# Optimization experiments

Hardware: AMD Instinct MI355X
Metric: run time of the kernel (lower is better)

The kernel has to match this reference:

```python
import jax, jax.numpy as jnp
import numpy as np

HIDDEN = 100  # hard-coded in the torch module


def setup_inputs() -> dict:
    key = jax.random.key(0)
    k1, k2, k3, k4, k5 = jax.random.split(key, 5)
    dims, N, M = 32, 4096, 8192
    centroids = jax.random.normal(k1, (N, dims), dtype=jnp.float32)
    x = jax.random.normal(k2, (M, dims), dtype=jnp.float32)
    # torch Linear params: y = x @ W.T (+ b)
    W1 = jax.random.normal(k3, (HIDDEN, dims), dtype=jnp.float32) / np.sqrt(dims)
    W2 = jax.random.normal(k4, (dims, HIDDEN), dtype=jnp.float32) / np.sqrt(HIDDEN)
    b2 = jax.random.uniform(k5, (dims,), dtype=jnp.float32, minval=-0.1, maxval=0.1)
    return {"centroids": centroids, "x": x, "W1": W1, "W2": W2, "b2": b2}


def reference(centroids, x, W1, W2, b2):
    dims = centroids.shape[1]
    # small MLP: Linear(dims,100,no bias) -> Linear(100,dims) -> tanh, then gate by centroids
    loc = jnp.tanh((centroids @ W1.T) @ W2.T + b2) * centroids  # [N, dims]
    # covariance = eye(dims) * var(centroids) (scalar, unbiased var over all elements)
    var = jnp.var(centroids, ddof=1)
    # diagonal-Gaussian log_prob, pairwise [N, M] via ||x-loc||^2 expansion (no NxMxD cube)
    sq = (
        jnp.sum(x * x, axis=1)[None, :]
        + jnp.sum(loc * loc, axis=1)[:, None]
        - 2.0 * (loc @ x.T)
    )  # [N, M]
    log_norm = dims * jnp.log(2.0 * jnp.pi * var)
    logp = -0.5 * (sq / var + log_norm)  # [N, M]
    return jnp.exp(logp).T  # [M, N]
```

## Files before the change

### kernel.cpp

```cpp
#include <hip/hip_runtime.h>
#include <math.h>

#define DIMS 32
#define NROWS 4096
#define MROWS 8192
#define HID 100
#define TS 128
#define LDK 132

#define L2E 1.44269504088896340736f

typedef float f32x4 __attribute__((ext_vector_type(4)));

__global__ __launch_bounds__(256) void k_init(const float* __restrict__ c,
                                              const float* __restrict__ W1,
                                              const float* __restrict__ W2,
                                              float* __restrict__ part,
                                              float* __restrict__ Mmat) {
    int b = blockIdx.x, t = threadIdx.x;
    const float4* c4 = (const float4*)c;
    float s = 0.0f, q = 0.0f;
    #pragma unroll
    for (int i = 0; i < 16; i++) {
        float4 a = c4[b * 4096 + i * 256 + t];
        s += a.x + a.y + a.z + a.w;
        q += a.x * a.x + a.y * a.y + a.z * a.z + a.w * a.w;
    }
    #pragma unroll
    for (int off = 32; off > 0; off >>= 1) {
        s += __shfl_down(s, off);
        q += __shfl_down(q, off);
    }
    __shared__ float red[8];
    int lane = t & 63, wid = t >> 6;
    if (lane == 0) { red[wid] = s; red[4 + wid] = q; }
    __syncthreads();
    if (t == 0) {
        part[2 * b]     = red[0] + red[1] + red[2] + red[3];
        part[2 * b + 1] = red[4] + red[5] + red[6] + red[7];
    }
    if (b == 0) {
        __shared__ float w1s[HID * DIMS];
        __shared__ float w2s[DIMS * HID];
        for (int i = t; i < HID * DIMS; i += 256) { w1s[i] = W1[i]; w2s[i] = W2[i]; }
        __syncthreads();
        #pragma unroll
        for (int o = 0; o < 4; o++) {
            int id = o * 256 + t;
            int r = id >> 5, cc = id & 31;
            float a = 0.0f;
            for (int j = 0; j < HID; j++) a += w2s[r * HID + j] * w1s[j * DIMS + cc];
            Mmat[id] = a;
        }
    }
}

__device__ __forceinline__ void load_var(const float* part, float& iv, float& var) {
    float S = 0.0f, Q = 0.0f;
    #pragma unroll
    for (int i = 0; i < 8; i++) { S += part[2 * i]; Q += part[2 * i + 1]; }
    const float cnt = (float)(NROWS * DIMS);
    var = (Q - S * S / cnt) / (cnt - 1.0f);
    iv = 1.0f / var;
}

__device__ __forceinline__ float tanh_fast(float x) {
    float xc = fminf(fmaxf(x, -10.0f), 10.0f);
    float e = __builtin_amdgcn_exp2f(xc * (2.0f * L2E));
    return (e - 1.0f) * __builtin_amdgcn_rcpf(e + 1.0f);
}

__global__ __launch_bounds__(256) void k_prep(const float* __restrict__ cent,
                                              const float* __restrict__ x,
                                              const float* __restrict__ b2,
                                              const float* __restrict__ part,
                                              const float* __restrict__ Mmat,
                                              float* __restrict__ loc,
                                              float* __restrict__ A,
                                              float* __restrict__ B) {
    float iv, var;
    load_var(part, iv, var);
    const float hv = -0.5f * L2E * iv;
    int t = threadIdx.x;

    if (blockIdx.x < 16) {
        __shared__ __align__(16) float ms[DIMS * DIMS];
        __shared__ float b2s[DIMS];
        for (int i = t; i < DIMS * DIMS; i += 256) ms[i] = Mmat[i];
        if (t < DIMS) b2s[t] = b2[t];
        __syncthreads();

        int n = blockIdx.x * 256 + t;
        float c[DIMS];
        const float4* cr = (const float4*)(cent + (size_t)n * DIMS);
        #pragma unroll
        for (int i = 0; i < 8; i++) {
            float4 v = cr[i];
            c[4 * i] = v.x; c[4 * i + 1] = v.y; c[4 * i + 2] = v.z; c[4 * i + 3] = v.w;
        }
        float lr[DIMS];
        float lsq = 0.0f;
        #pragma unroll
        for (int d = 0; d < DIMS; d++) {
            const float4* mr = (const float4*)&ms[d * DIMS];
            float a0 = 0.f, a1 = 0.f, a2 = 0.f, a3 = 0.f;
            #pragma unroll
            for (int kk = 0; kk < 8; kk++) {
                float4 m = mr[kk];
                a0 += c[4 * kk] * m.x;
                a1 += c[4 * kk + 1] * m.y;
                a2 += c[4 * kk + 2] * m.z;
                a3 += c[4 * kk + 3] * m.w;
            }
            float v = tanh_fast((a0 + a1) + (a2 + a3) + b2s[d]) * c[d];
            lr[d] = v;
            lsq += v * v;
        }
        float4* lo = (float4*)(loc + (size_t)n * DIMS);
        #pragma unroll
        for (int i = 0; i < 8; i++)
            lo[i] = make_float4(lr[4 * i], lr[4 * i + 1], lr[4 * i + 2], lr[4 * i + 3]);
        B[n] = hv * lsq;
    } else {
        int m = (blockIdx.x - 16) * 256 + t;
        const float4* xr = (const float4*)(x + (size_t)m * DIMS);
        float xsq = 0.0f;
        #pragma unroll
        for (int i = 0; i < 8; i++) {
            float4 v = xr[i];
            xsq += v.x * v.x + v.y * v.y + v.z * v.z + v.w * v.w;
        }
        float C0 = -16.0f * log2f(2.0f * (float)M_PI * var);
        A[m] = hv * xsq + C0;
    }
}

__global__ __launch_bounds__(256) void k_pair(const float* __restrict__ x,
                                              const float* __restrict__ loc,
                                              const float* __restrict__ A,
                                              const float* __restrict__ B,
                                              const float* __restrict__ part,
                                              float* __restrict__ out) {
    __shared__ __align__(16) float xs[DIMS][LDK];
    __shared__ __align__(16) float ls[DIMS][LDK];
    __shared__ float As[TS];
    __shared__ float Bs[TS];

    float iv, var;
    load_var(part, iv, var);
    const float s = L2E * iv;

    int n0 = blockIdx.x * TS;
    int m0 = blockIdx.y * TS;
    int t = threadIdx.x;

    {
        int ml = t >> 1;
        int kh = (t & 1) * 16;
        const float4* xr = (const float4*)(x + (size_t)(m0 + ml) * DIMS + kh);
        float4 v0 = xr[0], v1 = xr[1], v2 = xr[2], v3 = xr[3];
        float vv[16] = {v0.x, v0.y, v0.z, v0.w, v1.x, v1.y, v1.z, v1.w,
                        v2.x, v2.y, v2.z, v2.w, v3.x, v3.y, v3.z, v3.w};
        #pragma unroll
        for (int q = 0; q < 16; q++) xs[kh + q][ml] = vv[q];

        const float4* lr = (const float4*)(loc + (size_t)(n0 + ml) * DIMS + kh);
        float4 u0 = lr[0], u1 = lr[1], u2 = lr[2], u3 = lr[3];
        float uu[16] = {u0.x, u0.y, u0.z, u0.w, u1.x, u1.y, u1.z, u1.w,
                        u2.x, u2.y, u2.z, u2.w, u3.x, u3.y, u3.z, u3.w};
        #pragma unroll
        for (int q = 0; q < 16; q++) ls[kh + q][ml] = uu[q];
    }
    if (t < TS) As[t] = A[m0 + t];
    else        Bs[t - TS] = B[n0 + t - TS];
    __syncthreads();

    int tx = t & 15;
    int ty = t >> 4;

    float acc[8][8];
    #pragma unroll
    for (int i = 0; i < 8; i++)
        #pragma unroll
        for (int j = 0; j < 8; j++) acc[i][j] = 0.0f;

    #pragma unroll 4
    for (int k = 0; k < DIMS; k++) {
        float4 xa = *(const float4*)&xs[k][4 * ty];
        float4 xb = *(const float4*)&xs[k][64 + 4 * ty];
        float4 la = *(const float4*)&ls[k][4 * tx];
        float4 lb = *(const float4*)&ls[k][64 + 4 * tx];
        float xm[8] = {xa.x, xa.y, xa.z, xa.w, xb.x, xb.y, xb.z, xb.w};
        float ln[8] = {la.x, la.y, la.z, la.w, lb.x, lb.y, lb.z, lb.w};
        #pragma unroll
        for (int i = 0; i < 8; i++)
            #pragma unroll
            for (int j = 0; j < 8; j++)
                acc[i][j] += xm[i] * ln[j];
    }

    float ai[8], bj[8];
    #pragma unroll
    for (int i = 0; i < 4; i++) {
        ai[i] = As[4 * ty + i];
        ai[4 + i] = As[64 + 4 * ty + i];
    }
    #pragma unroll
    for (int j = 0; j < 4; j++) {
        bj[j] = Bs[4 * tx + j];
        bj[4 + j] = Bs[64 + 4 * tx + j];
    }

    #pragma unroll
    for (int i = 0; i < 8; i++) {
        int m = m0 + ((i < 4) ? (4 * ty + i) : (64 + 4 * ty + (i - 4)));
        f32x4 r0, r1;
        r0.x = __builtin_amdgcn_exp2f(fmaf(s, acc[i][0], ai[i] + bj[0]));
        r0.y = __builtin_amdgcn_exp2f(fmaf(s, acc[i][1], ai[i] + bj[1]));
        r0.z = __builtin_amdgcn_exp2f(fmaf(s, acc[i][2], ai[i] + bj[2]));
        r0.w = __builtin_amdgcn_exp2f(fmaf(s, acc[i][3], ai[i] + bj[3]));
        r1.x = __builtin_amdgcn_exp2f(fmaf(s, acc[i][4], ai[i] + bj[4]));
        r1.y = __builtin_amdgcn_exp2f(fmaf(s, acc[i][5], ai[i] + bj[5]));
        r1.z = __builtin_amdgcn_exp2f(fmaf(s, acc[i][6], ai[i] + bj[6]));
        r1.w = __builtin_amdgcn_exp2f(fmaf(s, acc[i][7], ai[i] + bj[7]));
        float* orow = out + (size_t)m * NROWS + n0;
        __builtin_nontemporal_store(r0, (f32x4*)&orow[4 * tx]);
        __builtin_nontemporal_store(r1, (f32x4*)&orow[64 + 4 * tx]);
    }
}

extern "C" void kernel_launch(void* const* d_in, const int* in_sizes, int n_in,
                              void* d_out, int out_size, void* d_ws, size_t ws_size,
                              hipStream_t stream) {
    const float* cent = (const float*)d_in[0];
    const float* x    = (const float*)d_in[1];
    const float* W1   = (const float*)d_in[2];
    const float* W2   = (const float*)d_in[3];
    const float* b2   = (const float*)d_in[4];
    float* out = (float*)d_out;

    float* ws   = (float*)d_ws;
    float* part = ws;
    float* Mmat = ws + 64;
    float* loc  = Mmat + 1024;
    float* A    = loc + NROWS * DIMS;
    float* B    = A + MROWS;

    k_init<<<8, 256, 0, stream>>>(cent, W1, W2, part, Mmat);
    k_prep<<<48, 256, 0, stream>>>(cent, x, b2, part, Mmat, loc, A, B);
    k_pair<<<dim3(NROWS / TS, MROWS / TS), 256, 0, stream>>>(x, loc, A, B, part, out);
}
```

Before: 176.0 us.

## Compute pairwise dot products with bf16 MFMA instead of fp32 FMA tiles

The prep kernel now writes x and loc as bf16 arrays. The pairwise kernel replaces the LDS-tiled fp32 outer-product loop with 16x16x32 bf16 MFMA instructions, loading fragments directly from global memory. Shared memory staging and the barrier are removed, and the output is written with per-element nontemporal stores. Rounding the inputs to bf16 reduces precision of the cross term inside the exponent, which may affect accuracy.

After: 178.3 us. About the same (+1.3%).

```diff
diff --git a/kernel.cpp b/kernel.cpp
--- a/kernel.cpp
+++ b/kernel.cpp
@@ -5,12 +5,11 @@
 #define NROWS 4096
 #define MROWS 8192
 #define HID 100
-#define TS 128
-#define LDK 132
 
 #define L2E 1.44269504088896340736f
 
 typedef float f32x4 __attribute__((ext_vector_type(4)));
+typedef short bf16x8 __attribute__((ext_vector_type(8)));
 
 __global__ __launch_bounds__(256) void k_init(const float* __restrict__ c,
                                               const float* __restrict__ W1,
@@ -70,14 +69,21 @@
     return (e - 1.0f) * __builtin_amdgcn_rcpf(e + 1.0f);
 }
 
+__device__ __forceinline__ unsigned short f2bf(float f) {
+    unsigned int u = __float_as_uint(f);
+    u += 0x7FFFu + ((u >> 16) & 1u);
+    return (unsigned short)(u >> 16);
+}
+
 __global__ __launch_bounds__(256) void k_prep(const float* __restrict__ cent,
                                               const float* __restrict__ x,
                                               const float* __restrict__ b2,
                                               const float* __restrict__ part,
                                               const float* __restrict__ Mmat,
-                                              float* __restrict__ loc,
                                               float* __restrict__ A,
-                                              float* __restrict__ B) {
+                                              float* __restrict__ B,
+                                              unsigned short* __restrict__ xb,
+                                              unsigned short* __restrict__ locb) {
     float iv, var;
     load_var(part, iv, var);
     const float hv = -0.5f * L2E * iv;
@@ -116,116 +122,93 @@
             lr[d] = v;
             lsq += v * v;
         }
-        float4* lo = (float4*)(loc + (size_t)n * DIMS);
-        #pragma unroll
-        for (int i = 0; i < 8; i++)
-            lo[i] = make_float4(lr[4 * i], lr[4 * i + 1], lr[4 * i + 2], lr[4 * i + 3]);
+        unsigned int w[16];
+        #pragma unroll
+        for (int d = 0; d < 16; d++)
+            w[d] = (unsigned int)f2bf(lr[2 * d]) | ((unsigned int)f2bf(lr[2 * d + 1]) << 16);
+        uint4* lo = (uint4*)(locb + (size_t)n * DIMS);
+        lo[0] = make_uint4(w[0], w[1], w[2], w[3]);
+        lo[1] = make_uint4(w[4], w[5], w[6], w[7]);
+        lo[2] = make_uint4(w[8], w[9], w[10], w[11]);
+        lo[3] = make_uint4(w[12], w[13], w[14], w[15]);
         B[n] = hv * lsq;
     } else {
         int m = (blockIdx.x - 16) * 256 + t;
         const float4* xr = (const float4*)(x + (size_t)m * DIMS);
         float xsq = 0.0f;
+        unsigned int w[16];
         #pragma unroll
         for (int i = 0; i < 8; i++) {
             float4 v = xr[i];
             xsq += v.x * v.x + v.y * v.y + v.z * v.z + v.w * v.w;
-        }
+            w[2 * i]     = (unsigned int)f2bf(v.x) | ((unsigned int)f2bf(v.y) << 16);
+            w[2 * i + 1] = (unsigned int)f2bf(v.z) | ((unsigned int)f2bf(v.w) << 16);
+        }
+        uint4* xo = (uint4*)(xb + (size_t)m * DIMS);
+        xo[0] = make_uint4(w[0], w[1], w[2], w[3]);
+        xo[1] = make_uint4(w[4], w[5], w[6], w[7]);
+        xo[2] = make_uint4(w[8], w[9], w[10], w[11]);
+        xo[3] = make_uint4(w[12], w[13], w[14], w[15]);
         float C0 = -16.0f * log2f(2.0f * (float)M_PI * var);
         A[m] = hv * xsq + C0;
     }
 }
 
-__global__ __launch_bounds__(256) void k_pair(const float* __restrict__ x,
-                                              const float* __restrict__ loc,
+__global__ __launch_bounds__(256) void k_pair(const unsigned short* __restrict__ xb,
+                                              const unsigned short* __restrict__ locb,
                                               const float* __restrict__ A,
                                               const float* __restrict__ B,
                                               const float* __restrict__ part,
                                               float* __restrict__ out) {
-    __shared__ __align__(16) float xs[DIMS][LDK];
-    __shared__ __align__(16) float ls[DIMS][LDK];
-    __shared__ float As[TS];
-    __shared__ float Bs[TS];
-
     float iv, var;
     load_var(part, iv, var);
     const float s = L2E * iv;
 
-    int n0 = blockIdx.x * TS;
-    int m0 = blockIdx.y * TS;
     int t = threadIdx.x;
-
-    {
-        int ml = t >> 1;
-        int kh = (t & 1) * 16;
-        const float4* xr = (const float4*)(x + (size_t)(m0 + ml) * DIMS + kh);
-        float4 v0 = xr[0], v1 = xr[1], v2 = xr[2], v3 = xr[3];
-        float vv[16] = {v0.x, v0.y, v0.z, v0.w, v1.x, v1.y, v1.z, v1.w,
-                        v2.x, v2.y, v2.z, v2.w, v3.x, v3.y, v3.z, v3.w};
-        #pragma unroll
-        for (int q = 0; q < 16; q++) xs[kh + q][ml] = vv[q];
-
-        const float4* lr = (const float4*)(loc + (size_t)(n0 + ml) * DIMS + kh);
-        float4 u0 = lr[0], u1 = lr[1], u2 = lr[2], u3 = lr[3];
-        float uu[16] = {u0.x, u0.y, u0.z, u0.w, u1.x, u1.y, u1.z, u1.w,
-                        u2.x, u2.y, u2.z, u2.w, u3.x, u3.y, u3.z, u3.w};
-        #pragma unroll
-        for (int q = 0; q < 16; q++) ls[kh + q][ml] = uu[q];
-    }
-    if (t < TS) As[t] = A[m0 + t];
-    else        Bs[t - TS] = B[n0 + t - TS];
-    __syncthreads();
-
-    int tx = t & 15;
-    int ty = t >> 4;
-
-    float acc[8][8];
-    #pragma unroll
-    for (int i = 0; i < 8; i++)
-        #pragma unroll
-        for (int j = 0; j < 8; j++) acc[i][j] = 0.0f;
-
-    #pragma unroll 4
-    for (int k = 0; k < DIMS; k++) {
-        float4 xa = *(const float4*)&xs[k][4 * ty];
-        float4 xb = *(const float4*)&xs[k][64 + 4 * ty];
-        float4 la = *(const float4*)&ls[k][4 * tx];
-        float4 lb = *(const float4*)&ls[k][64 + 4 * tx];
-        float xm[8] = {xa.x, xa.y, xa.z, xa.w, xb.x, xb.y, xb.z, xb.w};
-        float ln[8] = {la.x, la.y, la.z, la.w, lb.x, lb.y, lb.z, lb.w};
-        #pragma unroll
-        for (int i = 0; i < 8; i++)
+    int lane = t & 63, wid = t >> 6;
+    int m0 = blockIdx.y * 128 + (wid >> 1) * 64;
+    int n0 = blockIdx.x * 128 + (wid & 1) * 64;
+    int r = lane & 15, g = lane >> 4;
+
+    bf16x8 af[4], bfr[4];
+    #pragma unroll
+    for (int i = 0; i < 4; i++)
+        af[i] = *(const bf16x8*)(xb + (size_t)(m0 + 16 * i + r) * DIMS + 8 * g);
+    #pragma unroll
+    for (int j = 0; j < 4; j++)
+        bfr[j] = *(const bf16x8*)(locb + (size_t)(n0 + 16 * j + r) * DIMS + 8 * g);
+
+    f32x4 zero = {0.0f, 0.0f, 0.0f, 0.0f};
+    f32x4 acc[4][4];
+    #pragma unroll
+    for (int i = 0; i < 4; i++)
+        #pragma unroll
+        for (int j = 0; j < 4; j++)
+            acc[i][j] = __builtin_amdgcn_mfma_f32_16x16x32_bf16(af[i], bfr[j], zero, 0, 0, 0);
+
+    float Av[4][4];
+    #pragma unroll
+    for (int i = 0; i < 4; i++)
+        #pragma unroll
+        for (int q = 0; q < 4; q++)
+            Av[i][q] = A[m0 + 16 * i + 4 * g + q];
+    float Bv[4];
+    #pragma unroll
+    for (int j = 0; j < 4; j++)
+        Bv[j] = B[n0 + 16 * j + r];
+
+    #pragma unroll
+    for (int i = 0; i < 4; i++) {
+        #pragma unroll
+        for (int q = 0; q < 4; q++) {
+            float* orow = out + (size_t)(m0 + 16 * i + 4 * g + q) * NROWS + n0 + r;
+            float aq = Av[i][q];
             #pragma unroll
-            for (int j = 0; j < 8; j++)
-                acc[i][j] += xm[i] * ln[j];
-    }
-
-    float ai[8], bj[8];
-    #pragma unroll
-    for (int i = 0; i < 4; i++) {
-        ai[i] = As[4 * ty + i];
-        ai[4 + i] = As[64 + 4 * ty + i];
-    }
-    #pragma unroll
-    for (int j = 0; j < 4; j++) {
-        bj[j] = Bs[4 * tx + j];
-        bj[4 + j] = Bs[64 + 4 * tx + j];
-    }
-
-    #pragma unroll
-    for (int i = 0; i < 8; i++) {
-        int m = m0 + ((i < 4) ? (4 * ty + i) : (64 + 4 * ty + (i - 4)));
-        f32x4 r0, r1;
-        r0.x = __builtin_amdgcn_exp2f(fmaf(s, acc[i][0], ai[i] + bj[0]));
-        r0.y = __builtin_amdgcn_exp2f(fmaf(s, acc[i][1], ai[i] + bj[1]));
-        r0.z = __builtin_amdgcn_exp2f(fmaf(s, acc[i][2], ai[i] + bj[2]));
-        r0.w = __builtin_amdgcn_exp2f(fmaf(s, acc[i][3], ai[i] + bj[3]));
-        r1.x = __builtin_amdgcn_exp2f(fmaf(s, acc[i][4], ai[i] + bj[4]));
-        r1.y = __builtin_amdgcn_exp2f(fmaf(s, acc[i][5], ai[i] + bj[5]));
-        r1.z = __builtin_amdgcn_exp2f(fmaf(s, acc[i][6], ai[i] + bj[6]));
-        r1.w = __builtin_amdgcn_exp2f(fmaf(s, acc[i][7], ai[i] + bj[7]));
-        float* orow = out + (size_t)m * NROWS + n0;
-        __builtin_nontemporal_store(r0, (f32x4*)&orow[4 * tx]);
-        __builtin_nontemporal_store(r1, (f32x4*)&orow[64 + 4 * tx]);
+            for (int j = 0; j < 4; j++) {
+                float v = __builtin_amdgcn_exp2f(fmaf(s, acc[i][j][q], aq + Bv[j]));
+                __builtin_nontemporal_store(v, orow + 16 * j);
+            }
+        }
     }
 }
 
@@ -242,11 +225,12 @@
     float* ws   = (float*)d_ws;
     float* part = ws;
     float* Mmat = ws + 64;
-    float* loc  = Mmat + 1024;
-    float* A    = loc + NROWS * DIMS;
+    float* A    = Mmat + 1024;
     float* B    = A + MROWS;
+    unsigned short* xb   = (unsigned short*)(B + NROWS);
+    unsigned short* locb = xb + (size_t)MROWS * DIMS;
 
     k_init<<<8, 256, 0, stream>>>(cent, W1, W2, part, Mmat);
-    k_prep<<<48, 256, 0, stream>>>(cent, x, b2, part, Mmat, loc, A, B);
-    k_pair<<<dim3(NROWS / TS, MROWS / TS), 256, 0, stream>>>(x, loc, A, B, part, out);
-}
+    k_prep<<<48, 256, 0, stream>>>(cent, x, b2, part, Mmat, A, B, xb, locb);
+    k_pair<<<dim3(NROWS / 128, MROWS / 128), 256, 0, stream>>>(xb, locb, A, B, part, out);
+}
```
